# Performance work log

Measured on AMD Instinct MI355X. Metric: run time of the kernel, lower is better.

## Reference

```python
import jax, jax.numpy as jnp
import numpy as np

N_HEAD, D_MODEL, D_HEAD = 16, 1024, 64
QLEN, MLEN, BSZ = 1024, 1024, 4
KLEN = QLEN + MLEN
RLEN = KLEN
LN_EPS = 1e-5


def setup_inputs() -> dict:
    key = jax.random.key(0)
    ks = jax.random.split(key, 12)
    s = 0.02
    query = jax.random.normal(ks[0], (QLEN, BSZ, D_MODEL), jnp.float32)
    content = jax.random.normal(ks[1], (QLEN, BSZ, D_MODEL), jnp.float32)
    mems = jax.random.normal(ks[2], (MLEN, BSZ, D_MODEL), jnp.float32)
    r = jax.random.normal(ks[3], (RLEN, D_MODEL), jnp.float32)
    # causal mask with memory offset: query i may attend keys j <= i + MLEN
    i = jnp.arange(QLEN)[:, None]
    j = jnp.arange(KLEN)[None, :]
    attn_mask = (j > i + MLEN)[:, :, None]  # [qlen, klen, 1] bool, True = masked
    Wq = jax.random.normal(ks[4], (D_MODEL, N_HEAD * D_HEAD), jnp.float32) * s
    Wk = jax.random.normal(ks[5], (D_MODEL, N_HEAD * D_HEAD), jnp.float32) * s
    Wv = jax.random.normal(ks[6], (D_MODEL, N_HEAD * D_HEAD), jnp.float32) * s
    Wr = jax.random.normal(ks[7], (D_MODEL, N_HEAD * D_HEAD), jnp.float32) * s
    Wo = jax.random.normal(ks[8], (N_HEAD * D_HEAD, D_MODEL), jnp.float32) * s
    r_w_bias = jax.random.normal(ks[9], (N_HEAD, D_HEAD), jnp.float32) * s
    r_r_bias = jax.random.normal(ks[10], (N_HEAD, D_HEAD), jnp.float32) * s
    ln_gamma = jnp.ones((D_MODEL,), jnp.float32)
    ln_beta = jnp.zeros((D_MODEL,), jnp.float32)
    return dict(query=query, content=content, r=r, mems=mems, attn_mask=attn_mask,
                Wq=Wq, Wk=Wk, Wv=Wv, Wr=Wr, Wo=Wo,
                r_w_bias=r_w_bias, r_r_bias=r_r_bias,
                ln_gamma=ln_gamma, ln_beta=ln_beta)


def _rel_shift(x, cut_len):
    # x: [qlen, rlen, bsz, n_head]
    q, rl, b, n = x.shape
    zero_pad = jnp.zeros((q, 1, b, n), x.dtype)
    xp = jnp.concatenate([zero_pad, x], axis=1)          # [q, rl+1, b, n]
    xp = xp.reshape(rl + 1, q, b, n)[1:].reshape(q, rl, b, n)
    return xp[:, :cut_len]


def _layer_norm(x, gamma, beta):
    mu = jnp.mean(x, axis=-1, keepdims=True)
    var = jnp.mean(jnp.square(x - mu), axis=-1, keepdims=True)
    return (x - mu) * jax.lax.rsqrt(var + LN_EPS) * gamma + beta


def reference(query, content, r, mems, attn_mask, Wq, Wk, Wv, Wr, Wo,
              r_w_bias, r_r_bias, ln_gamma, ln_beta):
    qlen, bsz = query.shape[0], query.shape[1]
    cat = jnp.concatenate([mems, content], axis=0)        # [klen, b, d_model]
    klen = cat.shape[0]
    scale = 1.0 / (D_HEAD ** 0.5)

    w_head_q = (query @ Wq).reshape(qlen, bsz, N_HEAD, D_HEAD)
    w_head_k = (cat @ Wk).reshape(klen, bsz, N_HEAD, D_HEAD)
    w_head_v = (cat @ Wv).reshape(klen, bsz, N_HEAD, D_HEAD)
    r_head_k = (r @ Wr).reshape(-1, N_HEAD, D_HEAD)       # [rlen, n, d]

    AC = jnp.einsum('ibnd,jbnd->ijbn', w_head_q + r_w_bias, w_head_k)
    BD = jnp.einsum('ibnd,jnd->ijbn', w_head_q + r_r_bias, r_head_k)
    BD = _rel_shift(BD, cut_len=klen)

    attn_score = (AC + BD) * scale                        # [q, k, b, n]
    attn_score = jnp.where(attn_mask[:, :, :, None], jnp.float32(-1e30), attn_score)
    attn_prob = jax.nn.softmax(attn_score, axis=1)

    attn_vec = jnp.einsum('ijbn,jbnd->ibnd', attn_prob, w_head_v)
    attn_vec = attn_vec.reshape(qlen, bsz, N_HEAD * D_HEAD)
    attn_out = attn_vec @ Wo                              # [q, b, d_model]

    out = _layer_norm(query + attn_out, ln_gamma, ln_beta)
    return out
```

## Files before the change

kernel.cpp:

```cpp
#include <hip/hip_runtime.h>
#include <cstdint>
#include <cstddef>

constexpr int QLEN = 1024, MLEN = 1024, KLEN = 2048, RLEN = 2048;
constexpr int BSZ = 4, NH = 16, DH = 64, DM = 1024;

typedef __attribute__((ext_vector_type(8))) short bf16x8_t;
typedef __attribute__((ext_vector_type(4))) float f32x4_t;

#define DEV __device__ __forceinline__

DEV float b2f(unsigned short u) {
    union { unsigned x; float f; } v; v.x = ((unsigned)u) << 16; return v.f;
}
DEV unsigned short f2b(float f) {
    unsigned x = __float_as_uint(f);
    unsigned r = (x + 0x7fffu + ((x >> 16) & 1u)) >> 16;
    return (unsigned short)r;
}
DEV unsigned pack2(float lo, float hi) {
    return (unsigned)f2b(lo) | ((unsigned)f2b(hi) << 16);
}
DEV unsigned cvtpk(float lo, float hi) {
    unsigned r;
    asm("v_cvt_pk_bf16_f32 %0, %1, %2" : "=v"(r) : "v"(lo), "v"(hi));
    return r;
}
DEV void gl16(const unsigned short* g, unsigned short* l) {
    __builtin_amdgcn_global_load_lds(
        (const __attribute__((address_space(1))) unsigned int*)(const void*)g,
        (__attribute__((address_space(3))) unsigned int*)(void*)l, 16, 0, 0);
}

__global__ __launch_bounds__(256) void conv_bf16(const float* __restrict__ q,
                                                 const float* __restrict__ mems,
                                                 const float* __restrict__ content,
                                                 unsigned short* __restrict__ Qb,
                                                 unsigned short* __restrict__ catb) {
    const int which = blockIdx.y;
    const float* s = which == 0 ? q : (which == 1 ? mems : content);
    unsigned short* d = which == 0 ? Qb : (which == 1 ? catb : catb + (size_t)4096 * DM);
    size_t i = ((size_t)blockIdx.x * 256 + threadIdx.x) * 8;
    float4 f0 = *(const float4*)(s + i);
    float4 f1 = *(const float4*)(s + i + 4);
    uint4 pk;
    pk.x = pack2(f0.x, f0.y); pk.y = pack2(f0.z, f0.w);
    pk.z = pack2(f1.x, f1.y); pk.w = pack2(f1.z, f1.w);
    *(uint4*)(d + i) = pk;
}

__global__ __launch_bounds__(256) void transW_all(const float* __restrict__ Wq,
                                                  const float* __restrict__ Wk,
                                                  const float* __restrict__ Wv,
                                                  const float* __restrict__ Wr,
                                                  const float* __restrict__ Wo,
                                                  unsigned short* __restrict__ WqT,
                                                  unsigned short* __restrict__ WkvT,
                                                  unsigned short* __restrict__ WrT,
                                                  unsigned short* __restrict__ WoT) {
    const int z = blockIdx.z;
    const float* W = z == 0 ? Wq : z == 1 ? Wk : z == 2 ? Wv : z == 3 ? Wr : Wo;
    unsigned short* WT = z == 0 ? WqT : z == 1 ? WkvT
                       : z == 2 ? WkvT + (size_t)1024 * 1024 : z == 3 ? WrT : WoT;
    __shared__ float t[32][33];
    const int tx = threadIdx.x & 31, ty = threadIdx.x >> 5;
    const int n0 = blockIdx.x * 32, k0 = blockIdx.y * 32;
#pragma unroll
    for (int r = 0; r < 32; r += 8)
        t[ty + r][tx] = W[(size_t)(k0 + ty + r) * DM + n0 + tx];
    __syncthreads();
#pragma unroll
    for (int r = 0; r < 32; r += 8)
        WT[(size_t)(n0 + ty + r) * DM + k0 + tx] = f2b(t[tx][ty + r]);
}

__global__ __launch_bounds__(256) void gemm_proj(const unsigned short* __restrict__ Qb,
                                                 const unsigned short* __restrict__ catb,
                                                 const float* __restrict__ r_in,
                                                 const unsigned short* __restrict__ WqT,
                                                 const unsigned short* __restrict__ WkvT,
                                                 const unsigned short* __restrict__ WrT,
                                                 unsigned short* __restrict__ Qp,
                                                 unsigned short* __restrict__ Kp,
                                                 unsigned short* __restrict__ VT,
                                                 unsigned short* __restrict__ Rp) {
    constexpr int K = DM;
    const int bx = blockIdx.x;
    int seg, loc, gx;
    const unsigned short* BT;
    if (bx < 256)       { seg = 0; loc = bx;        gx = 8;  BT = WqT; }
    else if (bx < 1280) { seg = 1; loc = bx - 256;  gx = 16; BT = WkvT; }
    else                { seg = 2; loc = bx - 1280; gx = 8;  BT = WrT; }
    const int m0 = (loc / gx) * 128, n0 = (loc % gx) * 128;
    const bool isV = (seg == 1) && (n0 >= 1024);
    const int vb = m0 >> 11, vj0 = m0 & 2047;

    __shared__ unsigned short As[128 * 64];
    __shared__ unsigned short Bs[128 * 64];

    const int tid = threadIdx.x;
    const int wave = tid >> 6, lane = tid & 63;
    const int quad = lane >> 4, l16 = lane & 15;
    const int wm = (wave >> 1) * 64, wn = (wave & 1) * 64;
    const int ls = lane >> 3, l8 = lane & 7;
    const int sg = l8 ^ (ls & 7);
    const int swz7 = l16 & 15 & 7;

    const unsigned short* abase = (seg == 0) ? Qb : catb;

    f32x4_t acc[4][4] = {};

    for (int it = 0; it < K / 64; it++) {
        const int k0 = it * 64;

#pragma unroll
        for (int c = 0; c < 4; c++) {
            int cb = wave * 4 + c;
            int row = cb * 8 + ls;
            gl16(BT + (size_t)(n0 + row) * K + k0 + sg * 8, &Bs[cb * 512]);
        }
        if (seg != 2) {
#pragma unroll
            for (int c = 0; c < 4; c++) {
                int ca = wave * 4 + c;
                int row = ca * 8 + ls;
                size_t ar = isV ? (size_t)((vj0 + row) * 4 + vb) * K
                                : (size_t)(m0 + row) * K;
                gl16(abase + ar + k0 + sg * 8, &As[ca * 512]);
            }
        } else {
            const int srow = tid >> 1, hk = tid & 1;
            const float* ap = r_in + (size_t)(m0 + srow) * K + k0 + hk * 32;
#pragma unroll
            for (int c = 0; c < 4; c++) {
                float4 f0 = *(const float4*)(ap + c * 8);
                float4 f1 = *(const float4*)(ap + c * 8 + 4);
                uint4 pk;
                pk.x = pack2(f0.x, f0.y); pk.y = pack2(f0.z, f0.w);
                pk.z = pack2(f1.x, f1.y); pk.w = pack2(f1.z, f1.w);
                int slot = (hk * 4 + c) ^ (srow & 7);
                *(uint4*)((char*)As + srow * 128 + slot * 16) = pk;
            }
        }
        __syncthreads();

#pragma unroll
        for (int h = 0; h < 2; h++) {
            bf16x8_t af[4], bfr[4];
#pragma unroll
            for (int s = 0; s < 4; s++) {
                int arow = wm + s * 16 + l16;
                int brow = wn + s * 16 + l16;
                af[s]  = *(const bf16x8_t*)((const char*)As + arow * 128 + (((h * 4 + quad) ^ swz7) << 4));
                bfr[s] = *(const bf16x8_t*)((const char*)Bs + brow * 128 + (((h * 4 + quad) ^ swz7) << 4));
            }
#pragma unroll
            for (int sm = 0; sm < 4; sm++)
#pragma unroll
                for (int sn = 0; sn < 4; sn++)
                    acc[sm][sn] = __builtin_amdgcn_mfma_f32_16x16x32_bf16(af[sm], bfr[sn], acc[sm][sn], 0, 0, 0);
        }
        __syncthreads();
    }

#pragma unroll
    for (int sm = 0; sm < 4; sm++)
#pragma unroll
        for (int sn = 0; sn < 4; sn++) {
            if (isV) {
                int j = vj0 + wm + sm * 16 + quad * 4;
                int d = (n0 - 1024) + wn + sn * 16 + l16;
                uint2 pk;
                pk.x = pack2(acc[sm][sn][0], acc[sm][sn][1]);
                pk.y = pack2(acc[sm][sn][2], acc[sm][sn][3]);
                *(uint2*)(VT + ((size_t)(vb * DM + d)) * KLEN + j) = pk;
            } else {
#pragma unroll
                for (int rg = 0; rg < 4; rg++) {
                    int row = m0 + wm + sm * 16 + quad * 4 + rg;
                    int col = n0 + wn + sn * 16 + l16;
                    unsigned short v = f2b(acc[sm][sn][rg]);
                    if (seg == 0)      Qp[(size_t)row * 1024 + col] = v;
                    else if (seg == 2) Rp[(size_t)row * 1024 + col] = v;
                    else               Kp[(size_t)row * 1024 + col] = v;
                }
            }
        }
}

__global__ __launch_bounds__(256) void attn_flash(const unsigned short* __restrict__ Qp,
                                                  const unsigned short* __restrict__ Kp,
                                                  const unsigned short* __restrict__ VT,
                                                  const unsigned short* __restrict__ Rp,
                                                  const float* __restrict__ rwb,
                                                  const float* __restrict__ rrb,
                                                  unsigned short* __restrict__ O0,
                                                  unsigned short* __restrict__ O1,
                                                  float* __restrict__ lsum) {
    const int n = blockIdx.x, b = blockIdx.y;
    const int s = blockIdx.z & 1;
    const int i0 = (7 - (blockIdx.z >> 1)) * 128;
    const int tid = threadIdx.x;
    const int wave = tid >> 6, lane = tid & 63;
    const int l16 = lane & 15, quad = lane >> 4;
    const int ib = i0 + wave * 32;

    __shared__ unsigned short kvr[320 * 64];
    __shared__ unsigned short sbuf[4][2][16 * 88];

    const int swz = (l16 & 7) * 8;
    const int soA = (quad * 8) ^ swz;
    const int soB = (quad * 8 + 32) ^ swz;

    const int str = tid >> 3, sslot = tid & 7;
    const int wso = (sslot ^ (str & 7)) * 8;

    const float SCL = 0.18033688011112042f;

    bf16x8_t qac[2][2], qbd[2][2];
#pragma unroll
    for (int g = 0; g < 2; g++) {
        const unsigned short* qrow = Qp + ((size_t)((ib + g * 16 + l16) * BSZ + b)) * DM + n * DH;
#pragma unroll
        for (int kb = 0; kb < 2; kb++) {
            int off = kb * 32 + quad * 8;
            union { uint4 u4; unsigned short us[8]; } in;
            in.u4 = *(const uint4*)(qrow + off);
            union { bf16x8_t v; unsigned short us[8]; } oa, ob;
#pragma unroll
            for (int t = 0; t < 8; t++) {
                float q = b2f(in.us[t]);
                oa.us[t] = f2b((q + rwb[n * DH + off + t]) * SCL);
                ob.us[t] = f2b((q + rrb[n * DH + off + t]) * SCL);
            }
            qac[g][kb] = oa.v; qbd[g][kb] = ob.v;
        }
    }

    f32x4_t accO[2][4] = {};
    float l_i[2][4] = {};

    const unsigned short* vsrc0 = VT + ((size_t)(b * DM + n * DH)) * KLEN + sslot * 8;
    const unsigned short* rsrc0 = Rp + n * DH + sslot * 8;

    const int jtB = ((i0 + 96 + 31 + MLEN) >> 6) + 1;
    for (int jt = s; jt < jtB; jt += 2) {
        const int jb = jt * 64;
        const int pmin = jb - i0 + 896;

#pragma unroll
        for (int c = 0; c < 10; c++) {
            const int row = c * 32 + str;
            const unsigned short* src;
            if (c < 2) {
                src = Kp + ((size_t)((jb + row) * BSZ + b)) * DM + n * DH + sslot * 8;
            } else if (c < 4) {
                src = vsrc0 + (size_t)(row - 64) * KLEN + jb;
            } else {
                int p = pmin + (row - 128);
                p = p < 2047 ? p : 2047;
                src = rsrc0 + (size_t)p * DM;
            }
            *(uint4*)&kvr[(row << 6) + wso] = *(const uint4*)src;
        }
        __syncthreads();

        if (jb <= ib + 31 + MLEN) {
            const int pb_rel = 96 - 32 * wave;

#pragma unroll
            for (int h = 0; h < 2; h++) {
                f32x4_t accB[2][3] = {};
#pragma unroll
                for (int t3 = 0; t3 < 3; t3++) {
                    int rrow = 128 + pb_rel + (h * 3 + t3) * 16 + l16;
                    bf16x8_t r0 = *(const bf16x8_t*)&kvr[(rrow << 6) + soA];
                    bf16x8_t r1 = *(const bf16x8_t*)&kvr[(rrow << 6) + soB];
                    accB[0][t3] = __builtin_amdgcn_mfma_f32_16x16x32_bf16(qbd[0][0], r0, accB[0][t3], 0, 0, 0);
                    accB[0][t3] = __builtin_amdgcn_mfma_f32_16x16x32_bf16(qbd[0][1], r1, accB[0][t3], 0, 0, 0);
                    accB[1][t3] = __builtin_amdgcn_mfma_f32_16x16x32_bf16(qbd[1][0], r0, accB[1][t3], 0, 0, 0);
                    accB[1][t3] = __builtin_amdgcn_mfma_f32_16x16x32_bf16(qbd[1][1], r1, accB[1][t3], 0, 0, 0);
                }
#pragma unroll
                for (int t3 = 0; t3 < 3; t3++) {
                    int t = h * 3 + t3;
                    int rowb = quad * 4;
#pragma unroll
                    for (int g = 0; g < 2; g++) {
                        if (g == 0 ? (t >= 1) : (t <= 4)) {
                            unsigned lo = cvtpk(accB[g][t3][0], accB[g][t3][1]);
                            unsigned hi = cvtpk(accB[g][t3][2], accB[g][t3][3]);
                            int base = (g == 0 ? (t - 1) : t) * 16 + l16;
                            sbuf[wave][g][(rowb + 0) * 88 + base] = (unsigned short)lo;
                            sbuf[wave][g][(rowb + 1) * 88 + base] = (unsigned short)(lo >> 16);
                            sbuf[wave][g][(rowb + 2) * 88 + base] = (unsigned short)hi;
                            sbuf[wave][g][(rowb + 3) * 88 + base] = (unsigned short)(hi >> 16);
                        }
                    }
                }
            }

            float pprev[2][4];
#pragma unroll
            for (int nt = 0; nt < 4; nt++) {
                int krow = nt * 16 + l16;
                bf16x8_t k0 = *(const bf16x8_t*)&kvr[(krow << 6) + soA];
                bf16x8_t k1 = *(const bf16x8_t*)&kvr[(krow << 6) + soB];
                f32x4_t aS0 = {}, aS1 = {};
                aS0 = __builtin_amdgcn_mfma_f32_16x16x32_bf16(qac[0][0], k0, aS0, 0, 0, 0);
                aS0 = __builtin_amdgcn_mfma_f32_16x16x32_bf16(qac[0][1], k1, aS0, 0, 0, 0);
                aS1 = __builtin_amdgcn_mfma_f32_16x16x32_bf16(qac[1][0], k0, aS1, 0, 0, 0);
                aS1 = __builtin_amdgcn_mfma_f32_16x16x32_bf16(qac[1][1], k1, aS1, 0, 0, 0);

                if (nt > 0) {
                    int col = (nt - 1) * 16 + l16, rowb = quad * 4;
#pragma unroll
                    for (int g = 0; g < 2; g++) {
                        unsigned lo = cvtpk(pprev[g][0], pprev[g][1]);
                        unsigned hi = cvtpk(pprev[g][2], pprev[g][3]);
                        sbuf[wave][g][(rowb + 0) * 88 + col] = (unsigned short)lo;
                        sbuf[wave][g][(rowb + 1) * 88 + col] = (unsigned short)(lo >> 16);
                        sbuf[wave][g][(rowb + 2) * 88 + col] = (unsigned short)hi;
                        sbuf[wave][g][(rowb + 3) * 88 + col] = (unsigned short)(hi >> 16);
                    }
                }

                if (jb + 63 <= ib + MLEN) {
#pragma unroll
                    for (int g = 0; g < 2; g++)
#pragma unroll
                        for (int r = 0; r < 4; r++) {
                            int irow = quad * 4 + r;
                            float sc = (g ? aS1 : aS0)[r]
                                     + b2f(sbuf[wave][g][irow * 88 + nt * 16 + l16 - irow + 15]);
                            float e = __builtin_amdgcn_exp2f(sc);
                            l_i[g][r] += e;
                            pprev[g][r] = e;
                        }
                } else {
#pragma unroll
                    for (int g = 0; g < 2; g++)
#pragma unroll
                        for (int r = 0; r < 4; r++) {
                            int irow = quad * 4 + r;
                            float sc = (g ? aS1 : aS0)[r]
                                     + b2f(sbuf[wave][g][irow * 88 + nt * 16 + l16 - irow + 15]);
                            bool ok = (jb + nt * 16 + l16) <= (ib + g * 16 + irow + MLEN);
                            float e = ok ? __builtin_amdgcn_exp2f(sc) : 0.f;
                            l_i[g][r] += e;
                            pprev[g][r] = e;
                        }
                }
            }
            {
                int col = 48 + l16, rowb = quad * 4;
#pragma unroll
                for (int g = 0; g < 2; g++) {
                    unsigned lo = cvtpk(pprev[g][0], pprev[g][1]);
                    unsigned hi = cvtpk(pprev[g][2], pprev[g][3]);
                    sbuf[wave][g][(rowb + 0) * 88 + col] = (unsigned short)lo;
                    sbuf[wave][g][(rowb + 1) * 88 + col] = (unsigned short)(lo >> 16);
                    sbuf[wave][g][(rowb + 2) * 88 + col] = (unsigned short)hi;
                    sbuf[wave][g][(rowb + 3) * 88 + col] = (unsigned short)(hi >> 16);
                }
            }

#pragma unroll
            for (int kb2 = 0; kb2 < 2; kb2++) {
                bf16x8_t pf0 = *(const bf16x8_t*)&sbuf[wave][0][l16 * 88 + kb2 * 32 + quad * 8];
                bf16x8_t pf1 = *(const bf16x8_t*)&sbuf[wave][1][l16 * 88 + kb2 * 32 + quad * 8];
#pragma unroll
                for (int nt = 0; nt < 4; nt++) {
                    int vrow = 64 + nt * 16 + l16;
                    bf16x8_t vf = *(const bf16x8_t*)&kvr[(vrow << 6) + (kb2 ? soB : soA)];
                    accO[0][nt] = __builtin_amdgcn_mfma_f32_16x16x32_bf16(pf0, vf, accO[0][nt], 0, 0, 0);
                    accO[1][nt] = __builtin_amdgcn_mfma_f32_16x16x32_bf16(pf1, vf, accO[1][nt], 0, 0, 0);
                }
            }
        }
        __syncthreads();
    }

#pragma unroll
    for (int g = 0; g < 2; g++)
#pragma unroll
        for (int r = 0; r < 4; r++)
#pragma unroll
            for (int off = 1; off < 16; off <<= 1)
                l_i[g][r] += __shfl_xor(l_i[g][r], off);

    unsigned short* Op = s ? O1 : O0;
#pragma unroll
    for (int g = 0; g < 2; g++)
#pragma unroll
        for (int r = 0; r < 4; r++) {
            int irow = ib + g * 16 + quad * 4 + r;
            int rowlin = irow * BSZ + b;
            unsigned short* orow = Op + (size_t)rowlin * DM + n * DH;
#pragma unroll
            for (int nt = 0; nt < 4; nt++)
                orow[nt * 16 + l16] = f2b(accO[g][nt][r]);
            if (l16 == 0)
                lsum[((size_t)(s * 4096) + rowlin) * NH + n] = l_i[g][r];
        }
}

__global__ __launch_bounds__(256) void merge_part(const unsigned short* __restrict__ O0,
                                                  const unsigned short* __restrict__ O1,
                                                  const float* __restrict__ lsum,
                                                  unsigned short* __restrict__ AV) {
    const int row = blockIdx.x;
    const int d = threadIdx.x * 4;
    const int n = d >> 6;
    float l0 = lsum[(size_t)row * NH + n];
    float l1 = lsum[((size_t)4096 + row) * NH + n];
    float inv = 1.0f / (l0 + l1);
    size_t idx = (size_t)row * DM + d;
    unsigned short a[4], bb[4], res[4];
    *(uint2*)a  = *(const uint2*)(O0 + idx);
    *(uint2*)bb = *(const uint2*)(O1 + idx);
#pragma unroll
    for (int k = 0; k < 4; k++) res[k] = f2b((b2f(a[k]) + b2f(bb[k])) * inv);
    *(uint2*)(AV + idx) = *(uint2*)res;
}

__global__ __launch_bounds__(256) void gemm_wo(const unsigned short* __restrict__ A,
                                               const unsigned short* __restrict__ BT,
                                               unsigned short* __restrict__ C) {
    constexpr int K = DM, N = DM;
    __shared__ unsigned short As[128][72];
    __shared__ unsigned short Bs[64][72];

    const int tid = threadIdx.x;
    const int wave = tid >> 6, lane = tid & 63;
    const int quad = lane >> 4, l16 = lane & 15;
    const int m0 = blockIdx.y * 128, n0 = blockIdx.x * 64;
    const int wm = (wave >> 1) * 64, wn = (wave & 1) * 32;
    const int srow = tid >> 1, skk = (tid & 1) * 32;
    const int srB = tid >> 2, skB = (tid & 3) * 16;

    f32x4_t acc[4][2] = {};
    uint4 ar[4], br[2];

    auto prefetch = [&](int k0) {
        const unsigned short* ap = A + (size_t)(m0 + srow) * K + k0 + skk;
#pragma unroll
        for (int c = 0; c < 4; c++) ar[c] = *(const uint4*)(ap + c * 8);
        const unsigned short* bp = BT + (size_t)(n0 + srB) * K + k0 + skB;
#pragma unroll
        for (int c = 0; c < 2; c++) br[c] = *(const uint4*)(bp + c * 8);
    };

    prefetch(0);
    for (int it = 0; it < K / 64; it++) {
        __syncthreads();
#pragma unroll
        for (int c = 0; c < 4; c++) *(uint4*)&As[srow][skk + c * 8] = ar[c];
#pragma unroll
        for (int c = 0; c < 2; c++) *(uint4*)&Bs[srB][skB + c * 8] = br[c];
        __syncthreads();
        if (it + 1 < K / 64) prefetch((it + 1) * 64);

#pragma unroll
        for (int kb = 0; kb < 64; kb += 32) {
            bf16x8_t af[4], bfr[2];
#pragma unroll
            for (int s = 0; s < 4; s++) af[s] = *(const bf16x8_t*)&As[wm + s * 16 + l16][kb + quad * 8];
#pragma unroll
            for (int s = 0; s < 2; s++) bfr[s] = *(const bf16x8_t*)&Bs[wn + s * 16 + l16][kb + quad * 8];
#pragma unroll
            for (int sm = 0; sm < 4; sm++)
#pragma unroll
                for (int sn = 0; sn < 2; sn++)
                    acc[sm][sn] = __builtin_amdgcn_mfma_f32_16x16x32_bf16(af[sm], bfr[sn], acc[sm][sn], 0, 0, 0);
        }
    }

#pragma unroll
    for (int sm = 0; sm < 4; sm++)
#pragma unroll
        for (int sn = 0; sn < 2; sn++)
#pragma unroll
            for (int rg = 0; rg < 4; rg++) {
                int row = m0 + wm + sm * 16 + quad * 4 + rg;
                int col = n0 + wn + sn * 16 + l16;
                C[(size_t)row * N + col] = f2b(acc[sm][sn][rg]);
            }
}

__global__ __launch_bounds__(256) void ln_kernel(const float* __restrict__ query,
                                                 const unsigned short* __restrict__ AO,
                                                 const float* __restrict__ gamma,
                                                 const float* __restrict__ beta,
                                                 float* __restrict__ out) {
    const int row = blockIdx.x;
    const int tid = threadIdx.x;
    __shared__ float redS[4], redQ[4];

    float x[4], s = 0.f, ss = 0.f;
#pragma unroll
    for (int c = 0; c < 4; c++) {
        int d = c * 256 + tid;
        float v = query[(size_t)row * DM + d] + b2f(AO[(size_t)row * DM + d]);
        x[c] = v; s += v; ss += v * v;
    }
#pragma unroll
    for (int off = 32; off; off >>= 1) { s += __shfl_xor(s, off); ss += __shfl_xor(ss, off); }
    int w = tid >> 6, lane = tid & 63;
    if (lane == 0) { redS[w] = s; redQ[w] = ss; }
    __syncthreads();
    s  = redS[0] + redS[1] + redS[2] + redS[3];
    ss = redQ[0] + redQ[1] + redQ[2] + redQ[3];
    float mu  = s * (1.0f / DM);
    float var = ss * (1.0f / DM) - mu * mu;
    float inv = rsqrtf(var + 1e-5f);
#pragma unroll
    for (int c = 0; c < 4; c++) {
        int d = c * 256 + tid;
        out[(size_t)row * DM + d] = (x[c] - mu) * inv * gamma[d] + beta[d];
    }
}

extern "C" void kernel_launch(void* const* d_in, const int* in_sizes, int n_in,
                              void* d_out, int out_size, void* d_ws, size_t ws_size,
                              hipStream_t stream) {
    const float* query   = (const float*)d_in[0];
    const float* content = (const float*)d_in[1];
    const float* r_in    = (const float*)d_in[2];
    const float* mems    = (const float*)d_in[3];
    const float* Wq  = (const float*)d_in[5];
    const float* Wk  = (const float*)d_in[6];
    const float* Wv  = (const float*)d_in[7];
    const float* Wr  = (const float*)d_in[8];
    const float* Wo  = (const float*)d_in[9];
    const float* rwb = (const float*)d_in[10];
    const float* rrb = (const float*)d_in[11];
    const float* gam = (const float*)d_in[12];
    const float* bet = (const float*)d_in[13];
    float* out = (float*)d_out;

    char* ws = (char*)d_ws;
    unsigned short* WqT  = (unsigned short*)(ws);
    unsigned short* WkvT = (unsigned short*)(ws + (2u  << 20));
    unsigned short* WrT  = (unsigned short*)(ws + (6u  << 20));
    unsigned short* WoT  = (unsigned short*)(ws + (8u  << 20));
    unsigned short* Qp   = (unsigned short*)(ws + (10u << 20));
    unsigned short* Kp   = (unsigned short*)(ws + (18u << 20));
    unsigned short* VT   = (unsigned short*)(ws + (34u << 20));
    unsigned short* Rp   = (unsigned short*)(ws + (50u << 20));
    unsigned short* Qb   = (unsigned short*)(ws + (54u << 20));
    float*          lsum = (float*)(ws);
    unsigned short* AV   = (unsigned short*)(ws + (10u << 20));
    unsigned short* AO   = (unsigned short*)(ws);

    unsigned short* catb = (unsigned short*)d_out;
    unsigned short* O0   = (unsigned short*)d_out;
    unsigned short* O1   = (unsigned short*)d_out + (size_t)4096 * DM;

    conv_bf16<<<dim3(2048, 3), 256, 0, stream>>>(query, mems, content, Qb, catb);
    transW_all<<<dim3(32, 32, 5), 256, 0, stream>>>(Wq, Wk, Wv, Wr, Wo,
                                                    WqT, WkvT, WrT, WoT);

    gemm_proj<<<dim3(1408), 256, 0, stream>>>(Qb, catb, r_in, WqT, WkvT, WrT,
                                              Qp, Kp, VT, Rp);

    attn_flash<<<dim3(NH, BSZ, 16), 256, 0, stream>>>(Qp, Kp, VT, Rp, rwb, rrb,
                                                      O0, O1, lsum);

    merge_part<<<dim3(4096), 256, 0, stream>>>(O0, O1, lsum, AV);
    gemm_wo<<<dim3(16, 32), 256, 0, stream>>>(AV, WoT, AO);
    ln_kernel<<<dim3(4096), 256, 0, stream>>>(query, AO, gam, bet, out);
}
```

Baseline: 393.2 us.

## Use direct global-to-LDS loads with XOR swizzle in attention and Wo GEMM

Replaces register-staged global loads followed by LDS stores with gl16 direct global-to-LDS transfers, in both the attention K/V/R tile staging and the output-projection GEMM. The Wo GEMM drops its padded LDS layout and register prefetch pipeline in favour of a 64-wide XOR-swizzled layout that avoids bank conflicts, with a barrier after each compute step. This cuts VGPR use and LDS write instructions, but gives up the explicit overlap of next-tile loads with MFMA compute in the GEMM. The attention R-row clamp to 2047 is also removed, which assumes the index never goes out of range.

```diff
diff --git a/kernel.cpp b/kernel.cpp
--- a/kernel.cpp
+++ b/kernel.cpp
@@ -103,8 +103,8 @@
     const int quad = lane >> 4, l16 = lane & 15;
     const int wm = (wave >> 1) * 64, wn = (wave & 1) * 64;
     const int ls = lane >> 3, l8 = lane & 7;
-    const int sg = l8 ^ (ls & 7);
-    const int swz7 = l16 & 15 & 7;
+    const int sg = l8 ^ ls;
+    const int swz7 = l16 & 7;
 
     const unsigned short* abase = (seg == 0) ? Qb : catb;
 
@@ -212,8 +212,9 @@
     const int soA = (quad * 8) ^ swz;
     const int soB = (quad * 8 + 32) ^ swz;
 
-    const int str = tid >> 3, sslot = tid & 7;
-    const int wso = (sslot ^ (str & 7)) * 8;
+    const int lrow8 = lane >> 3;
+    const int sg8 = ((lane & 7) ^ lrow8) * 8;
+    unsigned short* const stg = &kvr[(wave * 80) << 6];
 
     const float SCL = 0.18033688011112042f;
 
@@ -240,8 +241,8 @@
     f32x4_t accO[2][4] = {};
     float l_i[2][4] = {};
 
-    const unsigned short* vsrc0 = VT + ((size_t)(b * DM + n * DH)) * KLEN + sslot * 8;
-    const unsigned short* rsrc0 = Rp + n * DH + sslot * 8;
+    const unsigned short* const vsrc0 = VT + ((size_t)(b * DM + n * DH)) * KLEN;
+    const unsigned short* const rsrc0 = Rp + n * DH;
 
     const int jtB = ((i0 + 96 + 31 + MLEN) >> 6) + 1;
     for (int jt = s; jt < jtB; jt += 2) {
@@ -249,19 +250,17 @@
         const int pmin = jb - i0 + 896;
 
 #pragma unroll
-        for (int c = 0; c < 10; c++) {
-            const int row = c * 32 + str;
+        for (int i = 0; i < 10; i++) {
+            const int row = wave * 80 + i * 8 + lrow8;
             const unsigned short* src;
-            if (c < 2) {
-                src = Kp + ((size_t)((jb + row) * BSZ + b)) * DM + n * DH + sslot * 8;
-            } else if (c < 4) {
-                src = vsrc0 + (size_t)(row - 64) * KLEN + jb;
+            if (row < 64) {
+                src = Kp + ((size_t)((jb + row) * BSZ + b)) * DM + n * DH + sg8;
+            } else if (row < 128) {
+                src = vsrc0 + (size_t)(row - 64) * KLEN + jb + sg8;
             } else {
-                int p = pmin + (row - 128);
-                p = p < 2047 ? p : 2047;
-                src = rsrc0 + (size_t)p * DM;
-            }
-            *(uint4*)&kvr[(row << 6) + wso] = *(const uint4*)src;
+                src = rsrc0 + (size_t)(pmin + row - 128) * DM + sg8;
+            }
+            gl16(src, stg + (i << 9));
         }
         __syncthreads();
 
@@ -428,52 +427,51 @@
                                                const unsigned short* __restrict__ BT,
                                                unsigned short* __restrict__ C) {
     constexpr int K = DM, N = DM;
-    __shared__ unsigned short As[128][72];
-    __shared__ unsigned short Bs[64][72];
+    __shared__ unsigned short As[128 * 64];
+    __shared__ unsigned short Bs[64 * 64];
 
     const int tid = threadIdx.x;
     const int wave = tid >> 6, lane = tid & 63;
     const int quad = lane >> 4, l16 = lane & 15;
     const int m0 = blockIdx.y * 128, n0 = blockIdx.x * 64;
     const int wm = (wave >> 1) * 64, wn = (wave & 1) * 32;
-    const int srow = tid >> 1, skk = (tid & 1) * 32;
-    const int srB = tid >> 2, skB = (tid & 3) * 16;
+    const int ls = lane >> 3, l8 = lane & 7;
+    const int sg = l8 ^ ls;
+    const int swz7 = l16 & 7;
 
     f32x4_t acc[4][2] = {};
-    uint4 ar[4], br[2];
-
-    auto prefetch = [&](int k0) {
-        const unsigned short* ap = A + (size_t)(m0 + srow) * K + k0 + skk;
-#pragma unroll
-        for (int c = 0; c < 4; c++) ar[c] = *(const uint4*)(ap + c * 8);
-        const unsigned short* bp = BT + (size_t)(n0 + srB) * K + k0 + skB;
-#pragma unroll
-        for (int c = 0; c < 2; c++) br[c] = *(const uint4*)(bp + c * 8);
-    };
-
-    prefetch(0);
+
     for (int it = 0; it < K / 64; it++) {
+        const int k0 = it * 64;
+
+#pragma unroll
+        for (int c = 0; c < 4; c++) {
+            int rb = wave * 32 + c * 8;
+            gl16(A + (size_t)(m0 + rb + ls) * K + k0 + sg * 8, &As[rb * 64]);
+        }
+#pragma unroll
+        for (int c = 0; c < 2; c++) {
+            int rb = wave * 16 + c * 8;
+            gl16(BT + (size_t)(n0 + rb + ls) * K + k0 + sg * 8, &Bs[rb * 64]);
+        }
         __syncthreads();
-#pragma unroll
-        for (int c = 0; c < 4; c++) *(uint4*)&As[srow][skk + c * 8] = ar[c];
-#pragma unroll
-        for (int c = 0; c < 2; c++) *(uint4*)&Bs[srB][skB + c * 8] = br[c];
-        __syncthreads();
-        if (it + 1 < K / 64) prefetch((it + 1) * 64);
-
-#pragma unroll
-        for (int kb = 0; kb < 64; kb += 32) {
+
+#pragma unroll
+        for (int h = 0; h < 2; h++) {
             bf16x8_t af[4], bfr[2];
 #pragma unroll
-            for (int s = 0; s < 4; s++) af[s] = *(const bf16x8_t*)&As[wm + s * 16 + l16][kb + quad * 8];
-#pragma unroll
-            for (int s = 0; s < 2; s++) bfr[s] = *(const bf16x8_t*)&Bs[wn + s * 16 + l16][kb + quad * 8];
+            for (int s = 0; s < 4; s++)
+                af[s] = *(const bf16x8_t*)((const char*)As + (wm + s * 16 + l16) * 128 + (((h * 4 + quad) ^ swz7) << 4));
+#pragma unroll
+            for (int s = 0; s < 2; s++)
+                bfr[s] = *(const bf16x8_t*)((const char*)Bs + (wn + s * 16 + l16) * 128 + (((h * 4 + quad) ^ swz7) << 4));
 #pragma unroll
             for (int sm = 0; sm < 4; sm++)
 #pragma unroll
                 for (int sn = 0; sn < 2; sn++)
                     acc[sm][sn] = __builtin_amdgcn_mfma_f32_16x16x32_bf16(af[sm], bfr[sn], acc[sm][sn], 0, 0, 0);
         }
+        __syncthreads();
     }
 
 #pragma unroll
```

After: 340.4 us. 1.16x faster.
